# Kernel tuning notes

Measured on AMD Instinct MI355X. Metric: run time of the kernel, lower is better.

## Reference

```python
import jax, jax.numpy as jnp
import numpy as np

N_NODES_TOTAL = 61440   # B*30
NODES = 30              # per-graph node count (forced by view(-1, 30*128))
E = 491520
IN_CH = 12
CHANS = [128, 512, 128]
KSIZE = 3
FC_OUT = 72             # 12 * 6


def setup_inputs() -> dict:
    key = jax.random.key(0)
    ks = jax.random.split(key, 24)
    d = {}
    d['x'] = jax.random.normal(ks[0], (N_NODES_TOTAL, IN_CH), dtype=jnp.float32)
    d['edge_index'] = jax.random.randint(ks[1], (2, E), 0, N_NODES_TOTAL, dtype=jnp.int64)
    # GCNConv(12, 12): PyG Linear weight [out, in] + bias
    d['gcn_w'] = jax.random.normal(ks[2], (12, 12), dtype=jnp.float32) * (1.0 / np.sqrt(12))
    d['gcn_b'] = jnp.zeros((12,), dtype=jnp.float32)
    # TCN: 3 TemporalBlocks, each uses conv1 (k=3, dilated causal) + 1x1 downsample
    in_c = IN_CH
    for i, out_c in enumerate(CHANS):
        d[f'conv_w{i}'] = jax.random.normal(ks[3 + 4 * i], (out_c, in_c, KSIZE), dtype=jnp.float32) * 0.01
        d[f'conv_b{i}'] = jnp.zeros((out_c,), dtype=jnp.float32)
        d[f'down_w{i}'] = jax.random.normal(ks[4 + 4 * i], (out_c, in_c, 1), dtype=jnp.float32) * 0.01
        d[f'down_b{i}'] = jnp.zeros((out_c,), dtype=jnp.float32)
        in_c = out_c
    d['fc_w'] = jax.random.normal(ks[20], (FC_OUT, CHANS[-1] * NODES), dtype=jnp.float32) * (1.0 / np.sqrt(CHANS[-1] * NODES))
    d['fc_b'] = jnp.zeros((FC_OUT,), dtype=jnp.float32)
    return d


def gcn_conv(x, edge_index, w, b):
    # PyG GCNConv: h = x W^T, add self-loops, sym normalize, scatter-add, + bias
    n = x.shape[0]
    h = x @ w.T
    loop = jnp.arange(n, dtype=edge_index.dtype)
    src = jnp.concatenate([edge_index[0], loop])
    dst = jnp.concatenate([edge_index[1], loop])
    deg = jax.ops.segment_sum(jnp.ones(src.shape[0], dtype=h.dtype), dst, num_segments=n)
    dinv = jnp.where(deg > 0, jax.lax.rsqrt(deg), 0.0)
    norm = dinv[src] * dinv[dst]                       # [E+N]
    out = jax.ops.segment_sum(norm[:, None] * h[src], dst, num_segments=n)
    return out + b


def causal_conv1d(x, w, b, dilation):
    # torch Conv1d(pad=(k-1)*d both sides) + Chomp1d((k-1)*d) == left-pad causal conv
    k = w.shape[-1]
    pad = (k - 1) * dilation
    y = jax.lax.conv_general_dilated(
        x, w, window_strides=(1,), padding=[(pad, 0)],
        rhs_dilation=(dilation,), dimension_numbers=('NCH', 'OIH', 'NCH'))
    return y + b[None, :, None]


def reference(x, edge_index, gcn_w, gcn_b,
              conv_w0, conv_b0, down_w0, down_b0,
              conv_w1, conv_b1, down_w1, down_b1,
              conv_w2, conv_b2, down_w2, down_b2,
              fc_w, fc_b):
    X = gcn_conv(x, edge_index, gcn_w, gcn_b)          # [B*30, 12]
    X = X.reshape(-1, NODES, IN_CH).transpose(0, 2, 1)  # [B, 12, 30]
    blocks = [(conv_w0, conv_b0, down_w0, down_b0),
              (conv_w1, conv_b1, down_w1, down_b1),
              (conv_w2, conv_b2, down_w2, down_b2)]
    for i, (cw, cb, dw, db) in enumerate(blocks):
        dil = 3 ** i
        out = jax.nn.relu(causal_conv1d(X, cw, cb, dil))
        res = causal_conv1d(X, dw, db, 1)              # 1x1 downsample (always in!=out here)
        X = jax.nn.relu(out + res)
    T = jax.nn.relu(X)                                  # [B, 128, 30]
    T = T.reshape(T.shape[0], -1)                       # [B, 3840], channel-major like torch flatten
    return T @ fc_w.T + fc_b                            # [B, 72]
```

## Files before the change

### kernel.cpp

```cpp
#include <hip/hip_runtime.h>
#include <hip/hip_bf16.h>

#define N_NODES 61440
#define NEDGE   491520
#define BATCH   2048
#define TT      30
#define C1      128
#define C2      512
#define C3      128
#define FCK     3840
#define MAXDEG  40

typedef float floatx16 __attribute__((ext_vector_type(16)));
typedef __bf16 bfrag   __attribute__((ext_vector_type(8)));

static __device__ __forceinline__ unsigned short f2bf(float f) {
    unsigned u = __float_as_uint(f);
    u = u + 0x7fffu + ((u >> 16) & 1u);
    return (unsigned short)(u >> 16);
}
static __device__ __forceinline__ bfrag ldf(const void* p) { return *(const bfrag*)p; }
#define MFMA(a, b, c) __builtin_amdgcn_mfma_f32_32x32x16_bf16(a, b, c, 0, 0, 0)

__global__ void k_edges_repack(
        const int* __restrict__ e32, int* __restrict__ cnt,
        unsigned short* __restrict__ eidx,
        const float* __restrict__ cw0, const float* __restrict__ dw0,
        const float* __restrict__ cw1, const float* __restrict__ dw1,
        const float* __restrict__ cw2, const float* __restrict__ dw2,
        const float* __restrict__ fcw,
        float* __restrict__ w0T, float* __restrict__ d0T,
        unsigned short* __restrict__ W1f, unsigned short* __restrict__ D1f,
        unsigned short* __restrict__ W2f, unsigned short* __restrict__ D2f,
        unsigned short* __restrict__ FCWf) {
    if (blockIdx.x < 1920) {
        int i = blockIdx.x * 256 + threadIdx.x;
        bool is64 = (e32[1] == 0) & (e32[3] == 0) & (e32[5] == 0) & (e32[7] == 0);
        int s, d;
        if (is64) { s = e32[2 * i]; d = e32[2 * (NEDGE + i)]; }
        else      { s = e32[i];     d = e32[NEDGE + i]; }
        int slot = atomicAdd(&cnt[d], 1);
        if (slot < MAXDEG) eidx[slot * N_NODES + d] = (unsigned short)s;
        return;
    }
    int i = (blockIdx.x - 1920) * 256 + threadIdx.x;
    if (i < 36 * 128) { int oc = i & 127, r = i >> 7; w0T[i] = cw0[oc * 36 + r]; }
    if (i < 12 * 128) { int oc = i & 127, ic = i >> 7; d0T[i] = dw0[oc * 12 + ic]; }
    if (i < 196608) {
        int pos = i & 511, f = i >> 9;
        int lane = pos >> 3, e = pos & 7;
        int oct = f & 15, q = (f >> 4) & 7, tap = f >> 7;
        int oc = oct * 32 + (lane & 31), ic = q * 16 + (lane >> 5) * 8 + e;
        W1f[i] = f2bf(cw1[(oc * 128 + ic) * 3 + tap]);
    } else if (i < 262144) {
        int j = i - 196608;
        int pos = j & 511, f = j >> 9;
        int lane = pos >> 3, e = pos & 7;
        int oct = f & 15, q = f >> 4;
        int oc = oct * 32 + (lane & 31), ic = q * 16 + (lane >> 5) * 8 + e;
        D1f[j] = f2bf(dw1[oc * 128 + ic]);
    } else if (i < 458752) {
        int j = i - 262144;
        int pos = j & 511, f = j >> 9;
        int lane = pos >> 3, e = pos & 7;
        int oct = f & 3, q = (f >> 2) & 31, tap = f >> 7;
        int oc = oct * 32 + (lane & 31), ic = q * 16 + (lane >> 5) * 8 + e;
        W2f[j] = f2bf(cw2[(oc * 512 + ic) * 3 + tap]);
    } else if (i < 524288) {
        int j = i - 458752;
        int pos = j & 511, f = j >> 9;
        int lane = pos >> 3, e = pos & 7;
        int oct = f & 3, q = f >> 2;
        int oc = oct * 32 + (lane & 31), ic = q * 16 + (lane >> 5) * 8 + e;
        D2f[j] = f2bf(dw2[oc * 512 + ic]);
    } else if (i < 892928) {
        int j = i - 524288;
        int pos = j & 511, f = j >> 9;
        int lane = pos >> 3, e = pos & 7;
        int oct = f % 3, q = f / 3;
        int o = oct * 32 + (lane & 31);
        int k = q * 16 + (lane >> 5) * 8 + e;
        float v = (o < 72) ? fcw[o * 3840 + (k & 127) * 30 + (k >> 7)] : 0.f;
        FCWf[j] = f2bf(v);
    }
}

__global__ __launch_bounds__(256) void k_block0(
        const float* __restrict__ x, const int* __restrict__ cnt,
        const unsigned short* __restrict__ eidx,
        const float* __restrict__ gw, const float* __restrict__ gb,
        const float* __restrict__ w0T, const float* __restrict__ d0T,
        const float* __restrict__ cb0, const float* __restrict__ db0,
        unsigned short* __restrict__ X1b) {
    __shared__ float wl[36 * 128];
    __shared__ float dl[12 * 128];
    __shared__ float cbl[128], dbl[128];
    __shared__ float gwl[144], gbl[12];
    __shared__ float aL[120][12];
    __shared__ float x0[4 * TT * 12];
    __shared__ __align__(16) unsigned short st[2][TT * 136];
    int tid = threadIdx.x;
    int b0 = blockIdx.x * 4;
    for (int i = tid; i < 36 * 128; i += 256) wl[i] = w0T[i];
    for (int i = tid; i < 12 * 128; i += 256) dl[i] = d0T[i];
    if (tid < 128) { cbl[tid] = cb0[tid]; dbl[tid] = db0[tid]; }
    if (tid < 144) gwl[tid] = gw[tid];
    if (tid >= 144 && tid < 156) gbl[tid - 144] = gb[tid - 144];

    {
        int th = tid & 127;
        int grp = tid >> 7;
        if (th < 120) {
            size_t n = (size_t)b0 * TT + th;
            int ne = cnt[n]; if (ne > MAXDEG) ne = MAXDEG;
            float a0 = 0.f, a1 = 0.f, a2 = 0.f, a3 = 0.f, a4 = 0.f, a5 = 0.f;
            for (int j = 0; j < ne; j++) {
                int s = eidx[j * N_NODES + n];
                float di = rsqrtf(1.0f + (float)cnt[s]);
                const float2* xp = (const float2*)(x + (size_t)s * 12 + grp * 6);
                float2 p0 = xp[0], p1 = xp[1], p2 = xp[2];
                a0 += di * p0.x; a1 += di * p0.y;
                a2 += di * p1.x; a3 += di * p1.y;
                a4 += di * p2.x; a5 += di * p2.y;
            }
            float* ap = &aL[th][grp * 6];
            ap[0] = a0; ap[1] = a1; ap[2] = a2; ap[3] = a3; ap[4] = a4; ap[5] = a5;
        }
    }
    __syncthreads();

    if (tid < 120) {
        size_t n = (size_t)b0 * TT + tid;
        float di = rsqrtf(1.0f + (float)cnt[n]);
        float d2 = di * di;
        const float4* xp = (const float4*)(x + n * 12);
        float u[12];
        #pragma unroll
        for (int q = 0; q < 3; q++) {
            float4 xv = xp[q];
            u[q*4+0] = di * aL[tid][q*4+0] + d2 * xv.x;
            u[q*4+1] = di * aL[tid][q*4+1] + d2 * xv.y;
            u[q*4+2] = di * aL[tid][q*4+2] + d2 * xv.z;
            u[q*4+3] = di * aL[tid][q*4+3] + d2 * xv.w;
        }
        #pragma unroll
        for (int c = 0; c < 12; c++) {
            float acc = gbl[c];
            #pragma unroll
            for (int j = 0; j < 12; j++) acc += u[j] * gwl[c * 12 + j];
            x0[tid * 12 + c] = acc;
        }
    }
    __syncthreads();

    int oc = tid & 127, half = tid >> 7;
    float cb = cbl[oc], db = dbl[oc];
    for (int bi = 0; bi < 2; bi++) {
        int bl = bi * 2 + half;
        const float* xb = x0 + bl * (TT * 12);
        float conv[TT], res[TT];
        #pragma unroll
        for (int t = 0; t < TT; t++) { conv[t] = 0.f; res[t] = 0.f; }
        #pragma unroll
        for (int ic = 0; ic < 12; ic++) {
            float w0v = wl[(ic * 3 + 0) * 128 + oc];
            float w1v = wl[(ic * 3 + 1) * 128 + oc];
            float w2v = wl[(ic * 3 + 2) * 128 + oc];
            float dv  = dl[ic * 128 + oc];
            #pragma unroll
            for (int t = 0; t < TT; t++) {
                float xv = xb[t * 12 + ic];
                conv[t] += w2v * xv;
                if (t + 1 < TT) conv[t + 1] += w1v * xv;
                if (t + 2 < TT) conv[t + 2] += w0v * xv;
                res[t] += dv * xv;
            }
        }
        #pragma unroll
        for (int t = 0; t < TT; t++) {
            float o1 = fmaxf(conv[t] + cb, 0.f);
            st[half][t * 136 + oc] = f2bf(fmaxf(o1 + res[t] + db, 0.f));
        }
        __syncthreads();
        for (int idx = tid; idx < 2 * TT * 16; idx += 256) {
            int h = idx / (TT * 16), rem = idx - h * (TT * 16);
            int row = rem >> 4, seg = rem & 15;
            *(uint4*)(X1b + (size_t)((b0 + bi * 2 + h) * TT + row) * 128 + seg * 8) =
                *(const uint4*)(&st[h][row * 136 + seg * 8]);
        }
        __syncthreads();
    }
}

__global__ __launch_bounds__(256, 2) void k_tcn12(
        const unsigned short* __restrict__ X1b,
        const unsigned short* __restrict__ W1f, const unsigned short* __restrict__ D1f,
        const float* __restrict__ cb1, const float* __restrict__ db1,
        const unsigned short* __restrict__ W2f, const unsigned short* __restrict__ D2f,
        const float* __restrict__ cb2, const float* __restrict__ db2,
        unsigned short* __restrict__ X3b) {
    __shared__ __align__(16) unsigned short X1l[61 * 136];
    __shared__ __align__(16) unsigned short X2l[61 * 520];
    const int tid  = threadIdx.x;
    const int lane = tid & 63;
    const int wave = tid >> 6;
    const int tcol = lane & 31;
    const int half = lane >> 5;
    const int b0 = blockIdx.x * 2;

    auto ldw1 = [&](bfrag* dst, int oct, int qc) {
        #pragma unroll
        for (int tap = 0; tap < 3; tap++)
            #pragma unroll
            for (int qq = 0; qq < 4; qq++)
                dst[tap * 4 + qq] =
                    ldf(W1f + (((tap * 8 + qc * 4 + qq) * 16 + oct) << 9) + lane * 8);
        #pragma unroll
        for (int qq = 0; qq < 4; qq++)
            dst[12 + qq] = ldf(D1f + (((qc * 4 + qq) * 16 + oct) << 9) + lane * 8);
    };
    auto ldw2 = [&](bfrag* dst, int oct, int qc) {
        #pragma unroll
        for (int tap = 0; tap < 3; tap++)
            #pragma unroll
            for (int qq = 0; qq < 4; qq++)
                dst[tap * 4 + qq] =
                    ldf(W2f + (((tap * 32 + qc * 4 + qq) * 4 + oct) << 9) + lane * 8);
        #pragma unroll
        for (int qq = 0; qq < 4; qq++)
            dst[12 + qq] = ldf(D2f + (((qc * 4 + qq) * 4 + oct) << 9) + lane * 8);
    };

    for (int idx = tid; idx < 960; idx += 256) {
        int row = idx >> 4, seg = idx & 15;
        *(uint4*)(X1l + row * 136 + seg * 8) =
            *(const uint4*)(X1b + ((size_t)(b0 * 30 + row) << 7) + seg * 8);
    }
    if (tid < 17) *(uint4*)(X1l + 60 * 136 + tid * 8) = make_uint4(0, 0, 0, 0);
    if (tid < 65) *(uint4*)(X2l + 60 * 520 + tid * 8) = make_uint4(0, 0, 0, 0);
    __syncthreads();

    {
        bfrag wf[2][16];
        ldw1(wf[0], wave, 0);
        floatx16 accc[2], accd[2];
        #pragma unroll
        for (int s = 0; s < 8; s++) {
            const int qc = s & 1;
            const int oct = (s >> 1) * 4 + wave;
            if (qc == 0) { accc[0] = 0; accc[1] = 0; accd[0] = 0; accd[1] = 0; }
            if (s < 7)
                ldw1(wf[(s + 1) & 1], ((s + 1) >> 1) * 4 + wave, (s + 1) & 1);
            #pragma unroll
            for (int bl = 0; bl < 2; bl++) {
                bfrag bx[3][4];
                #pragma unroll
                for (int si = 0; si < 3; si++) {
                    int trow = tcol - si * 3;
                    const unsigned short* rp = ((unsigned)trow < 30u)
                        ? (X1l + (bl * 30 + trow) * 136) : (X1l + 60 * 136);
                    #pragma unroll
                    for (int qq = 0; qq < 4; qq++)
                        bx[si][qq] = ldf(rp + (qc * 4 + qq) * 16 + half * 8);
                }
                #pragma unroll
                for (int qq = 0; qq < 4; qq++) {
                    accc[bl] = MFMA(wf[s & 1][8 + qq],  bx[0][qq], accc[bl]);
                    accc[bl] = MFMA(wf[s & 1][4 + qq],  bx[1][qq], accc[bl]);
                    accc[bl] = MFMA(wf[s & 1][qq],      bx[2][qq], accc[bl]);
                    accd[bl] = MFMA(wf[s & 1][12 + qq], bx[0][qq], accd[bl]);
                }
            }
            if (qc == 1 && tcol < 30) {
                #pragma unroll
                for (int bl = 0; bl < 2; bl++) {
                    unsigned short* wp = X2l + (bl * 30 + tcol) * 520 + oct * 32 + half * 4;
                    #pragma unroll
                    for (int gi = 0; gi < 4; gi++) {
                        int ocb = oct * 32 + half * 4 + gi * 8;
                        float4 cbv = *(const float4*)(cb1 + ocb);
                        float4 dbv = *(const float4*)(db1 + ocb);
                        float v0 = fmaxf(fmaxf(accc[bl][gi*4+0] + cbv.x, 0.f) + accd[bl][gi*4+0] + dbv.x, 0.f);
                        float v1 = fmaxf(fmaxf(accc[bl][gi*4+1] + cbv.y, 0.f) + accd[bl][gi*4+1] + dbv.y, 0.f);
                        float v2 = fmaxf(fmaxf(accc[bl][gi*4+2] + cbv.z, 0.f) + accd[bl][gi*4+2] + dbv.z, 0.f);
                        float v3 = fmaxf(fmaxf(accc[bl][gi*4+3] + cbv.w, 0.f) + accd[bl][gi*4+3] + dbv.w, 0.f);
                        unsigned p0 = (unsigned)f2bf(v0) | ((unsigned)f2bf(v1) << 16);
                        unsigned p1 = (unsigned)f2bf(v2) | ((unsigned)f2bf(v3) << 16);
                        *(uint2*)(wp + gi * 8) = make_uint2(p0, p1);
                    }
                }
            }
        }
    }
    __syncthreads();

    {
        const int oct = wave;
        bfrag wf[2][16];
        ldw2(wf[0], oct, 0);
        floatx16 accc[2], accd[2];
        accc[0] = 0; accc[1] = 0; accd[0] = 0; accd[1] = 0;
        #pragma unroll
        for (int qc = 0; qc < 8; qc++) {
            if (qc < 7) ldw2(wf[(qc + 1) & 1], oct, qc + 1);
            #pragma unroll
            for (int bl = 0; bl < 2; bl++) {
                bfrag bx[3][4];
                #pragma unroll
                for (int si = 0; si < 3; si++) {
                    int trow = tcol - si * 9;
                    const unsigned short* rp = ((unsigned)trow < 30u)
                        ? (X2l + (bl * 30 + trow) * 520) : (X2l + 60 * 520);
                    #pragma unroll
                    for (int qq = 0; qq < 4; qq++)
                        bx[si][qq] = ldf(rp + (qc * 4 + qq) * 16 + half * 8);
                }
                #pragma unroll
                for (int qq = 0; qq < 4; qq++) {
                    accc[bl] = MFMA(wf[qc & 1][8 + qq],  bx[0][qq], accc[bl]);
                    accc[bl] = MFMA(wf[qc & 1][4 + qq],  bx[1][qq], accc[bl]);
                    accc[bl] = MFMA(wf[qc & 1][qq],      bx[2][qq], accc[bl]);
                    accd[bl] = MFMA(wf[qc & 1][12 + qq], bx[0][qq], accd[bl]);
                }
            }
        }
        if (tcol < 30) {
            #pragma unroll
            for (int bl = 0; bl < 2; bl++) {
                unsigned short* wp = X1l + (bl * 30 + tcol) * 136 + oct * 32 + half * 4;
                #pragma unroll
                for (int gi = 0; gi < 4; gi++) {
                    int ocb = oct * 32 + half * 4 + gi * 8;
                    float4 cbv = *(const float4*)(cb2 + ocb);
                    float4 dbv = *(const float4*)(db2 + ocb);
                    float v0 = fmaxf(fmaxf(accc[bl][gi*4+0] + cbv.x, 0.f) + accd[bl][gi*4+0] + dbv.x, 0.f);
                    float v1 = fmaxf(fmaxf(accc[bl][gi*4+1] + cbv.y, 0.f) + accd[bl][gi*4+1] + dbv.y, 0.f);
                    float v2 = fmaxf(fmaxf(accc[bl][gi*4+2] + cbv.z, 0.f) + accd[bl][gi*4+2] + dbv.z, 0.f);
                    float v3 = fmaxf(fmaxf(accc[bl][gi*4+3] + cbv.w, 0.f) + accd[bl][gi*4+3] + dbv.w, 0.f);
                    unsigned p0 = (unsigned)f2bf(v0) | ((unsigned)f2bf(v1) << 16);
                    unsigned p1 = (unsigned)f2bf(v2) | ((unsigned)f2bf(v3) << 16);
                    *(uint2*)(wp + gi * 8) = make_uint2(p0, p1);
                }
            }
        }
    }
    __syncthreads();
    for (int idx = tid; idx < 960; idx += 256) {
        int row = idx >> 4, seg = idx & 15;
        *(uint4*)(X3b + ((size_t)(b0 * 30 + row) << 7) + seg * 8) =
            *(const uint4*)(X1l + row * 136 + seg * 8);
    }
}

__global__ __launch_bounds__(256) void k_fc_mfma(
        const unsigned short* __restrict__ X3b,
        const unsigned short* __restrict__ FCWf,
        unsigned short* __restrict__ P) {
    __shared__ __align__(16) unsigned short xt[128 * 248];
    const int tid  = threadIdx.x;
    const int lane = tid & 63;
    const int wave = tid >> 6;
    const int half = lane >> 5;
    const int bg = blockIdx.x & 15;
    const int kc = blockIdx.x >> 4;

    for (int idx = tid; idx < 128 * 32; idx += 256) {
        int row = idx >> 5, seg = idx & 31;
        if (seg < 30)
            *(uint4*)(xt + row * 248 + seg * 8) =
                *(const uint4*)(X3b + (size_t)(bg * 128 + row) * FCK + kc * 240 + seg * 8);
    }
    __syncthreads();

    const int bl = wave * 32 + (lane & 31);
    floatx16 acc[3];
    acc[0] = 0; acc[1] = 0; acc[2] = 0;
    #pragma unroll
    for (int ql = 0; ql < 15; ql++) {
        int q = kc * 15 + ql;
        bfrag bx = ldf(xt + bl * 248 + ql * 16 + half * 8);
        #pragma unroll
        for (int oct = 0; oct < 3; oct++) {
            bfrag af = ldf(FCWf + ((q * 3 + oct) << 9) + lane * 8);
            acc[oct] = MFMA(af, bx, acc[oct]);
        }
    }
    unsigned short* base = P + (size_t)kc * 96 * BATCH;
    const int b = bg * 128 + bl;
    #pragma unroll
    for (int oct = 0; oct < 3; oct++)
        #pragma unroll
        for (int j = 0; j < 16; j++) {
            int o = oct * 32 + half * 4 + (j >> 2) * 8 + (j & 3);
            base[(size_t)o * BATCH + b] = f2bf(acc[oct][j]);
        }
}

__global__ __launch_bounds__(256) void k_fc_reduce(
        const unsigned short* __restrict__ P, const float* __restrict__ fcb,
        float* __restrict__ out) {
    int j = blockIdx.x * blockDim.x + threadIdx.x;
    int o = j >> 11, b = j & 2047;
    float acc = fcb[o];
    #pragma unroll
    for (int kc = 0; kc < 16; kc++) {
        unsigned u = P[((size_t)kc * 96 + o) * BATCH + b];
        acc += __uint_as_float(u << 16);
    }
    out[b * 72 + o] = acc;
}


extern "C" void kernel_launch(void* const* d_in, const int* in_sizes, int n_in,
                              void* d_out, int out_size, void* d_ws, size_t ws_size,
                              hipStream_t stream) {
    const float* x   = (const float*)d_in[0];
    const int*   e32 = (const int*)  d_in[1];
    const float* gw  = (const float*)d_in[2];
    const float* gb  = (const float*)d_in[3];
    const float* cw0 = (const float*)d_in[4];
    const float* cb0 = (const float*)d_in[5];
    const float* dw0 = (const float*)d_in[6];
    const float* db0 = (const float*)d_in[7];
    const float* cw1 = (const float*)d_in[8];
    const float* cb1 = (const float*)d_in[9];
    const float* dw1 = (const float*)d_in[10];
    const float* db1 = (const float*)d_in[11];
    const float* cw2 = (const float*)d_in[12];
    const float* cb2 = (const float*)d_in[13];
    const float* dw2 = (const float*)d_in[14];
    const float* db2 = (const float*)d_in[15];
    const float* fcw = (const float*)d_in[16];
    const float* fcb = (const float*)d_in[17];

    char* w = (char*)d_ws;
    auto alloc = [&](size_t bytes) {
        char* p = w;
        w += (bytes + 255) & ~(size_t)255;
        return p;
    };
    int*            cnt  = (int*)           alloc(N_NODES * 4);
    unsigned short* eidx = (unsigned short*)alloc((size_t)N_NODES * MAXDEG * 2);
    float* w0T  = (float*)alloc(36 * 128 * 4);
    float* d0T  = (float*)alloc(12 * 128 * 4);
    unsigned short* W1f  = (unsigned short*)alloc(196608 * 2);
    unsigned short* D1f  = (unsigned short*)alloc(65536 * 2);
    unsigned short* W2f  = (unsigned short*)alloc(196608 * 2);
    unsigned short* D2f  = (unsigned short*)alloc(65536 * 2);
    unsigned short* FCWf = (unsigned short*)alloc(368640 * 2);
    unsigned short* X1b  = (unsigned short*)alloc((size_t)BATCH * TT * C1 * 2);
    unsigned short* X3b  = (unsigned short*)alloc((size_t)BATCH * TT * C3 * 2);
    unsigned short* P    = (unsigned short*)alloc((size_t)16 * 96 * BATCH * 2);

    hipMemsetAsync(cnt, 0, N_NODES * 4, stream);
    k_edges_repack<<<1920 + 3488, 256, 0, stream>>>(
        e32, cnt, eidx, cw0, dw0, cw1, dw1, cw2, dw2, fcw,
        w0T, d0T, W1f, D1f, W2f, D2f, FCWf);
    k_block0<<<BATCH / 4, 256, 0, stream>>>(x, cnt, eidx, gw, gb,
                                            w0T, d0T, cb0, db0, X1b);
    k_tcn12<<<BATCH / 2, 256, 0, stream>>>(X1b, W1f, D1f, cb1, db1,
                                           W2f, D2f, cb2, db2, X3b);
    k_fc_mfma<<<256, 256, 0, stream>>>(X3b, FCWf, P);
    k_fc_reduce<<<72 * BATCH / 256, 256, 0, stream>>>(P, fcb, (float*)d_out);
}
```

Before: 158.5 us.

## XOR-swizzle LDS activation tiles and prefetch first weight slice before staging

```diff
diff --git a/kernel.cpp b/kernel.cpp
--- a/kernel.cpp
+++ b/kernel.cpp
@@ -21,6 +21,7 @@
 }
 static __device__ __forceinline__ bfrag ldf(const void* p) { return *(const bfrag*)p; }
 #define MFMA(a, b, c) __builtin_amdgcn_mfma_f32_32x32x16_bf16(a, b, c, 0, 0, 0)
+#define SWZ(row, off) ((off) ^ (((row) & 7) << 3))
 
 __global__ void k_edges_repack(
         const int* __restrict__ e32, int* __restrict__ cnt,
@@ -231,9 +232,12 @@
             dst[12 + qq] = ldf(D2f + (((qc * 4 + qq) * 4 + oct) << 9) + lane * 8);
     };
 
+    bfrag wf[2][16];
+    ldw1(wf[0], wave, 0);
+
     for (int idx = tid; idx < 960; idx += 256) {
         int row = idx >> 4, seg = idx & 15;
-        *(uint4*)(X1l + row * 136 + seg * 8) =
+        *(uint4*)(X1l + row * 136 + SWZ(row, seg * 8)) =
             *(const uint4*)(X1b + ((size_t)(b0 * 30 + row) << 7) + seg * 8);
     }
     if (tid < 17) *(uint4*)(X1l + 60 * 136 + tid * 8) = make_uint4(0, 0, 0, 0);
@@ -241,8 +245,6 @@
     __syncthreads();
 
     {
-        bfrag wf[2][16];
-        ldw1(wf[0], wave, 0);
         floatx16 accc[2], accd[2];
         #pragma unroll
         for (int s = 0; s < 8; s++) {
@@ -257,11 +259,12 @@
                 #pragma unroll
                 for (int si = 0; si < 3; si++) {
                     int trow = tcol - si * 3;
-                    const unsigned short* rp = ((unsigned)trow < 30u)
-                        ? (X1l + (bl * 30 + trow) * 136) : (X1l + 60 * 136);
+                    int xr = ((unsigned)trow < 30u) ? (bl * 30 + trow) : 60;
+                    const unsigned short* rp = X1l + xr * 136;
+                    const int sw = (xr & 7) << 3;
                     #pragma unroll
                     for (int qq = 0; qq < 4; qq++)
-                        bx[si][qq] = ldf(rp + (qc * 4 + qq) * 16 + half * 8);
+                        bx[si][qq] = ldf(rp + (((qc * 4 + qq) * 16 + half * 8) ^ sw));
                 }
                 #pragma unroll
                 for (int qq = 0; qq < 4; qq++) {
@@ -274,7 +277,9 @@
             if (qc == 1 && tcol < 30) {
                 #pragma unroll
                 for (int bl = 0; bl < 2; bl++) {
-                    unsigned short* wp = X2l + (bl * 30 + tcol) * 520 + oct * 32 + half * 4;
+                    const int prow = bl * 30 + tcol;
+                    unsigned short* wp = X2l + prow * 520;
+                    const int sw = (prow & 7) << 3;
                     #pragma unroll
                     for (int gi = 0; gi < 4; gi++) {
                         int ocb = oct * 32 + half * 4 + gi * 8;
@@ -286,7 +291,7 @@
                         float v3 = fmaxf(fmaxf(accc[bl][gi*4+3] + cbv.w, 0.f) + accd[bl][gi*4+3] + dbv.w, 0.f);
                         unsigned p0 = (unsigned)f2bf(v0) | ((unsigned)f2bf(v1) << 16);
                         unsigned p1 = (unsigned)f2bf(v2) | ((unsigned)f2bf(v3) << 16);
-                        *(uint2*)(wp + gi * 8) = make_uint2(p0, p1);
+                        *(uint2*)(wp + ((oct * 32 + half * 4 + gi * 8) ^ sw)) = make_uint2(p0, p1);
                     }
                 }
             }
@@ -296,38 +301,41 @@
 
     {
         const int oct = wave;
-        bfrag wf[2][16];
-        ldw2(wf[0], oct, 0);
+        bfrag wf2[2][16];
+        ldw2(wf2[0], oct, 0);
         floatx16 accc[2], accd[2];
         accc[0] = 0; accc[1] = 0; accd[0] = 0; accd[1] = 0;
         #pragma unroll
         for (int qc = 0; qc < 8; qc++) {
-            if (qc < 7) ldw2(wf[(qc + 1) & 1], oct, qc + 1);
+            if (qc < 7) ldw2(wf2[(qc + 1) & 1], oct, qc + 1);
             #pragma unroll
             for (int bl = 0; bl < 2; bl++) {
                 bfrag bx[3][4];
                 #pragma unroll
                 for (int si = 0; si < 3; si++) {
                     int trow = tcol - si * 9;
-                    const unsigned short* rp = ((unsigned)trow < 30u)
-                        ? (X2l + (bl * 30 + trow) * 520) : (X2l + 60 * 520);
+                    int xr = ((unsigned)trow < 30u) ? (bl * 30 + trow) : 60;
+                    const unsigned short* rp = X2l + xr * 520;
+                    const int sw = (xr & 7) << 3;
                     #pragma unroll
                     for (int qq = 0; qq < 4; qq++)
-                        bx[si][qq] = ldf(rp + (qc * 4 + qq) * 16 + half * 8);
+                        bx[si][qq] = ldf(rp + (((qc * 4 + qq) * 16 + half * 8) ^ sw));
                 }
                 #pragma unroll
                 for (int qq = 0; qq < 4; qq++) {
-                    accc[bl] = MFMA(wf[qc & 1][8 + qq],  bx[0][qq], accc[bl]);
-                    accc[bl] = MFMA(wf[qc & 1][4 + qq],  bx[1][qq], accc[bl]);
-                    accc[bl] = MFMA(wf[qc & 1][qq],      bx[2][qq], accc[bl]);
-                    accd[bl] = MFMA(wf[qc & 1][12 + qq], bx[0][qq], accd[bl]);
+                    accc[bl] = MFMA(wf2[qc & 1][8 + qq],  bx[0][qq], accc[bl]);
+                    accc[bl] = MFMA(wf2[qc & 1][4 + qq],  bx[1][qq], accc[bl]);
+                    accc[bl] = MFMA(wf2[qc & 1][qq],      bx[2][qq], accc[bl]);
+                    accd[bl] = MFMA(wf2[qc & 1][12 + qq], bx[0][qq], accd[bl]);
                 }
             }
         }
         if (tcol < 30) {
             #pragma unroll
             for (int bl = 0; bl < 2; bl++) {
-                unsigned short* wp = X1l + (bl * 30 + tcol) * 136 + oct * 32 + half * 4;
+                const int prow = bl * 30 + tcol;
+                unsigned short* wp = X1l + prow * 136;
+                const int sw = (prow & 7) << 3;
                 #pragma unroll
                 for (int gi = 0; gi < 4; gi++) {
                     int ocb = oct * 32 + half * 4 + gi * 8;
@@ -339,7 +347,7 @@
                     float v3 = fmaxf(fmaxf(accc[bl][gi*4+3] + cbv.w, 0.f) + accd[bl][gi*4+3] + dbv.w, 0.f);
                     unsigned p0 = (unsigned)f2bf(v0) | ((unsigned)f2bf(v1) << 16);
                     unsigned p1 = (unsigned)f2bf(v2) | ((unsigned)f2bf(v3) << 16);
-                    *(uint2*)(wp + gi * 8) = make_uint2(p0, p1);
+                    *(uint2*)(wp + ((oct * 32 + half * 4 + gi * 8) ^ sw)) = make_uint2(p0, p1);
                 }
             }
         }
@@ -348,7 +356,7 @@
     for (int idx = tid; idx < 960; idx += 256) {
         int row = idx >> 4, seg = idx & 15;
         *(uint4*)(X3b + ((size_t)(b0 * 30 + row) << 7) + seg * 8) =
-            *(const uint4*)(X1l + row * 136 + seg * 8);
+            *(const uint4*)(X1l + row * 136 + SWZ(row, seg * 8));
     }
 }
 
```

Result: slower. 164.9 us (+4.1%).
